# Kernel optimization log

Measured on AMD Instinct MI355X. Metric: run time of the kernel, lower is better.

Reference implementation:

```python
import jax, jax.numpy as jnp
import numpy as np
import math

NUM_EMBED = 1024
EMBED_DIM = 256
COMMITMENT_COST = 0.25


def setup_inputs() -> dict:
    key = jax.random.key(0)
    k1, k2 = jax.random.split(key)
    inputs = jax.random.normal(k1, (16, EMBED_DIM, 4096), dtype=jnp.float32)
    embed = jax.random.normal(k2, (NUM_EMBED, EMBED_DIM), dtype=jnp.float32)
    return {"inputs": inputs, "embed": embed}


def reference(inputs, embed):
    sg = jax.lax.stop_gradient
    num_embed = embed.shape[0]
    # channels-first (B, D, T) -> (B, T, D)
    x = jnp.swapaxes(inputs, 1, -1)
    B, T, D = x.shape
    flat = x.reshape(-1, D)  # (N, D)
    # pairwise squared distances to the codebook: (N, K)
    d2 = (jnp.sum(flat * flat, axis=1, keepdims=True)
          + jnp.sum(embed * embed, axis=1)
          - 2.0 * flat @ embed.T)
    q_idx = jnp.argmin(d2, axis=1)  # (N,) int
    # one-hot @ embed is just a gather of the nearest codewords
    z_q = embed[q_idx].reshape(x.shape)  # (B, T, D)
    vq_loss = jnp.mean((z_q - sg(x)) ** 2)
    commitment_loss = jnp.mean((sg(z_q) - x) ** 2)
    loss = vq_loss + COMMITMENT_COST * commitment_loss
    # straight-through estimator
    z_q_st = x + sg(z_q - x)
    # codebook usage stats: probs = mean of the one-hot rows
    n = flat.shape[0]
    probs = jnp.zeros((num_embed,), dtype=flat.dtype).at[q_idx].add(1.0) / n
    perplexity = jnp.exp(-jnp.sum(probs * jnp.log(probs + 1e-10)))
    num_spatial_positions = n / B  # == T
    kldiv_r = (math.log(num_embed) * num_spatial_positions
               * jnp.ones((B, 1), dtype=x.dtype))
    z_q_out = jnp.swapaxes(z_q_st, 1, -1)  # back to (B, D, T)
    return z_q_out, loss, kldiv_r, perplexity
```

## Files before the change

kernel.cpp:

```cpp
#include <hip/hip_runtime.h>
#include <math.h>

#define T_DIM 4096
#define D_DIM 256
#define K_NUM 1024
#define B_NUM 16
#define N_TOT (B_NUM * T_DIM)
#define EPS_FLAG 0.03f

typedef short short8 __attribute__((ext_vector_type(8)));
typedef float f32x4 __attribute__((ext_vector_type(4)));

#define WS_FLAGCNT 0
#define WS_LOSS 4
#define WS_HIST 64
#define WS_E2 4352
#define WS_QIDX 8704
#define WS_FLAGLIST 270848
#define WS_ESWZ 540672

__device__ inline unsigned short bf16r(float v) {
    unsigned u = __float_as_uint(v);
    unsigned r = u + 0x7FFFu + ((u >> 16) & 1u);
    return (unsigned short)(r >> 16);
}

__device__ inline void gl_lds16(const void* g, void* l) {
    __builtin_amdgcn_global_load_lds(
        (const __attribute__((address_space(1))) unsigned int*)g,
        (__attribute__((address_space(3))) unsigned int*)l, 16, 0, 0);
}

__global__ __launch_bounds__(256) void e2_kernel(const float* __restrict__ embed,
                                                 float* __restrict__ e2) {
    const int wave = threadIdx.x >> 6;
    const int lane = threadIdx.x & 63;
    const int k = blockIdx.x * 4 + wave;
    const float4* row = (const float4*)(embed + (size_t)k * D_DIM);
    float4 v = row[lane];
    float s = v.x * v.x + v.y * v.y + v.z * v.z + v.w * v.w;
    #pragma unroll
    for (int off = 32; off; off >>= 1) s += __shfl_down(s, off);
    if (lane == 0) e2[k] = s;
}

__global__ __launch_bounds__(256) void prep_eswz_kernel(const float* __restrict__ embed,
                                                        unsigned char* __restrict__ eswz) {
    const int tau = blockIdx.x * 256 + threadIdx.x;
    const int g = tau >> 9;
    const int k = (tau >> 6) & 7;
    const int l = tau & 63;
    const int col = g * 16 + (l & 15);
    const int d0 = k * 32 + ((l >> 4) << 3);
    const float* src = embed + (size_t)col * D_DIM + d0;
    short8 hi, lo;
    #pragma unroll
    for (int j = 0; j < 8; ++j) {
        float v = src[j];
        unsigned short hs = bf16r(v);
        float hif = __uint_as_float((unsigned)hs << 16);
        unsigned short ls = bf16r(v - hif);
        hi[j] = (short)hs; lo[j] = (short)ls;
    }
    *(short8*)(eswz + (size_t)g * 16384 + k * 1024 + l * 16) = hi;
    *(short8*)(eswz + (size_t)g * 16384 + 8192 + k * 1024 + l * 16) = lo;
}

__global__ __launch_bounds__(256, 2) void argmin_mfma_kernel(
    const float* __restrict__ x, const unsigned char* __restrict__ eswz,
    const float* __restrict__ e2, int* __restrict__ qidx,
    int* __restrict__ flagcnt, int* __restrict__ flaglist)
{
    __shared__ __align__(16) unsigned char bbuf[2][32768];
    __shared__ float e2s[K_NUM];

    const int tid = threadIdx.x;
    const int w = tid >> 6;
    const int l = tid & 63;
    const int rb = blockIdx.x * 128;
    const int b = rb >> 12;
    const float* xb = x + (size_t)b * (D_DIM * T_DIM);

    {
        const unsigned char* src = eswz + (size_t)tid * 16;
        #pragma unroll
        for (int r = 0; r < 8; ++r) gl_lds16(src + r * 4096, &bbuf[0][tid * 16 + r * 4096]);
    }
    for (int i = tid; i < K_NUM; i += 256) e2s[i] = e2[i];

    short8 Ah[2][8], Al[2][8];
    #pragma unroll
    for (int f = 0; f < 2; ++f) {
        const int row = rb + w * 32 + f * 16 + (l & 15);
        const int t = row & (T_DIM - 1);
        const float* xp = xb + t;
        #pragma unroll
        for (int k = 0; k < 8; ++k) {
            const int d0 = k * 32 + ((l >> 4) << 3);
            short8 hi, lo;
            #pragma unroll
            for (int j = 0; j < 8; ++j) {
                float v = xp[(size_t)(d0 + j) * T_DIM];
                unsigned short hs = bf16r(v);
                float hif = __uint_as_float((unsigned)hs << 16);
                unsigned short ls = bf16r(v - hif);
                hi[j] = (short)hs; lo[j] = (short)ls;
            }
            Ah[f][k] = hi; Al[f][k] = lo;
        }
    }
    __syncthreads();

    float bestv[8], secv[8];
    int   besti[8];
    #pragma unroll
    for (int s = 0; s < 8; ++s) { bestv[s] = 3.4e38f; secv[s] = 3.4e38f; besti[s] = 0x7FFFFFFF; }

    for (int g = 0; g < 32; ++g) {
        if (g + 1 < 32) {
            const unsigned char* src = eswz + (size_t)(g + 1) * 32768 + (size_t)tid * 16;
            unsigned char* dst = &bbuf[(g + 1) & 1][tid * 16];
            #pragma unroll
            for (int r = 0; r < 8; ++r) gl_lds16(src + r * 4096, dst + r * 4096);
        }
        const unsigned char* bb = bbuf[g & 1];

        f32x4 a00 = {0.f,0.f,0.f,0.f}, a01 = {0.f,0.f,0.f,0.f};
        f32x4 a10 = {0.f,0.f,0.f,0.f}, a11 = {0.f,0.f,0.f,0.f};
        #pragma unroll
        for (int k = 0; k < 8; ++k) {
            short8 bh0 = *(const short8*)(bb + k * 1024 + l * 16);
            short8 bl0 = *(const short8*)(bb + 8192 + k * 1024 + l * 16);
            short8 bh1 = *(const short8*)(bb + 16384 + k * 1024 + l * 16);
            short8 bl1 = *(const short8*)(bb + 16384 + 8192 + k * 1024 + l * 16);
            a00 = __builtin_amdgcn_mfma_f32_16x16x32_bf16(Ah[0][k], bh0, a00, 0, 0, 0);
            a10 = __builtin_amdgcn_mfma_f32_16x16x32_bf16(Ah[1][k], bh0, a10, 0, 0, 0);
            a01 = __builtin_amdgcn_mfma_f32_16x16x32_bf16(Ah[0][k], bh1, a01, 0, 0, 0);
            a11 = __builtin_amdgcn_mfma_f32_16x16x32_bf16(Ah[1][k], bh1, a11, 0, 0, 0);
            a00 = __builtin_amdgcn_mfma_f32_16x16x32_bf16(Al[0][k], bh0, a00, 0, 0, 0);
            a10 = __builtin_amdgcn_mfma_f32_16x16x32_bf16(Al[1][k], bh0, a10, 0, 0, 0);
            a01 = __builtin_amdgcn_mfma_f32_16x16x32_bf16(Al[0][k], bh1, a01, 0, 0, 0);
            a11 = __builtin_amdgcn_mfma_f32_16x16x32_bf16(Al[1][k], bh1, a11, 0, 0, 0);
            a00 = __builtin_amdgcn_mfma_f32_16x16x32_bf16(Ah[0][k], bl0, a00, 0, 0, 0);
            a10 = __builtin_amdgcn_mfma_f32_16x16x32_bf16(Ah[1][k], bl0, a10, 0, 0, 0);
            a01 = __builtin_amdgcn_mfma_f32_16x16x32_bf16(Ah[0][k], bl1, a01, 0, 0, 0);
            a11 = __builtin_amdgcn_mfma_f32_16x16x32_bf16(Ah[1][k], bl1, a11, 0, 0, 0);
        }

        const int col0 = g * 32 + (l & 15);
        const float e2a = e2s[col0];
        const float e2b = e2s[col0 + 16];
        #pragma unroll
        for (int f = 0; f < 2; ++f) {
            const f32x4 accA = f ? a10 : a00;
            const f32x4 accB = f ? a11 : a01;
            #pragma unroll
            for (int r = 0; r < 4; ++r) {
                const int s = f * 4 + r;
                float sA = fmaf(-2.f, accA[r], e2a);
                float sB = fmaf(-2.f, accB[r], e2b);
                bool swp = sB < sA;
                float lo = swp ? sB : sA;
                float hi = swp ? sA : sB;
                int   li = swp ? col0 + 16 : col0;
                bool upd = lo < bestv[s];
                float mx = upd ? bestv[s] : lo;
                bestv[s] = upd ? lo : bestv[s];
                besti[s] = upd ? li : besti[s];
                secv[s] = fminf(secv[s], fminf(mx, hi));
            }
        }
        __syncthreads();
    }

    #pragma unroll
    for (int slot = 0; slot < 8; ++slot) {
        float bv = bestv[slot], sv = secv[slot];
        int bi = besti[slot];
        #pragma unroll
        for (int d = 1; d < 16; d <<= 1) {
            float ob = __shfl_xor(bv, d);
            int   oi = __shfl_xor(bi, d);
            float os = __shfl_xor(sv, d);
            bool take = (ob < bv) || (ob == bv && oi < bi);
            float loser = take ? bv : ob;
            bv = take ? ob : bv;
            bi = take ? oi : bi;
            sv = fminf(fminf(sv, os), loser);
        }
        if ((l & 15) == 0) {
            const int row = rb + w * 32 + (slot >> 2) * 16 + (l >> 4) * 4 + (slot & 3);
            qidx[row] = bi;
            if (sv - bv < EPS_FLAG) {
                int p = atomicAdd(flagcnt, 1);
                flaglist[p] = row;
            }
        }
    }
}

__global__ __launch_bounds__(256) void cleanup_kernel(
    const float* __restrict__ x, const float* __restrict__ embed,
    const float* __restrict__ e2, const int* __restrict__ flagcnt,
    const int* __restrict__ flaglist, int* __restrict__ qidx)
{
    __shared__ float xr[256];
    __shared__ float rv[256];
    __shared__ int   rix[256];
    const int tid = threadIdx.x;
    int cnt = flagcnt[0];
    if (cnt > N_TOT) cnt = N_TOT;
    for (int it = blockIdx.x; it < cnt; it += gridDim.x) {
        const int row = flaglist[it];
        const int b = row >> 12, t = row & (T_DIM - 1);
        __syncthreads();
        xr[tid] = x[(size_t)b * (D_DIM * T_DIM) + (size_t)tid * T_DIM + t];
        __syncthreads();
        float best = 3.4e38f; int bi = 0x7FFFFFFF;
        for (int q = 0; q < 4; ++q) {
            const int c = q * 256 + tid;
            const float4* ep = (const float4*)(embed + (size_t)c * D_DIM);
            float acc = 0.f;
            #pragma unroll 8
            for (int dd = 0; dd < 64; ++dd) {
                float4 ev = ep[dd];
                acc = fmaf(ev.x, xr[dd * 4 + 0], acc);
                acc = fmaf(ev.y, xr[dd * 4 + 1], acc);
                acc = fmaf(ev.z, xr[dd * 4 + 2], acc);
                acc = fmaf(ev.w, xr[dd * 4 + 3], acc);
            }
            const float s = e2[c] - 2.f * acc;
            if (s < best || (s == best && c < bi)) { best = s; bi = c; }
        }
        rv[tid] = best; rix[tid] = bi;
        __syncthreads();
        for (int off = 128; off; off >>= 1) {
            if (tid < off) {
                float ov = rv[tid + off]; int oi = rix[tid + off];
                if (ov < rv[tid] || (ov == rv[tid] && oi < rix[tid])) { rv[tid] = ov; rix[tid] = oi; }
            }
            __syncthreads();
        }
        if (tid == 0) qidx[row] = rix[0];
    }
}

__global__ __launch_bounds__(256) void gather_kernel(
    const float* __restrict__ x, const float* __restrict__ embed,
    const int* __restrict__ qidx, float* __restrict__ out,
    float* __restrict__ loss_sum, int* __restrict__ hist)
{
    const int tid = threadIdx.x;
    const int n = blockIdx.x * 256 + tid;
    const int b = n >> 12, t = n & (T_DIM - 1);
    const int d0 = blockIdx.y * 64;
    const int idx = qidx[n];
    if (blockIdx.y == 0) atomicAdd(&hist[idx], 1);

    const float4* ep = (const float4*)(embed + (size_t)idx * D_DIM + d0);
    const float* xp = x + (size_t)b * (D_DIM * T_DIM) + (size_t)d0 * T_DIM + t;
    float*       op = out + (size_t)b * (D_DIM * T_DIM) + (size_t)d0 * T_DIM + t;

    float local = 0.f;
    #pragma unroll 4
    for (int i = 0; i < 16; ++i) {
        const float4 ev = ep[i];
        const size_t dd = (size_t)i * 4;
        float xv0 = xp[(dd + 0) * T_DIM];
        float xv1 = xp[(dd + 1) * T_DIM];
        float xv2 = xp[(dd + 2) * T_DIM];
        float xv3 = xp[(dd + 3) * T_DIM];
        op[(dd + 0) * T_DIM] = ev.x;
        op[(dd + 1) * T_DIM] = ev.y;
        op[(dd + 2) * T_DIM] = ev.z;
        op[(dd + 3) * T_DIM] = ev.w;
        float f0 = ev.x - xv0, f1 = ev.y - xv1, f2 = ev.z - xv2, f3 = ev.w - xv3;
        local = fmaf(f0, f0, local);
        local = fmaf(f1, f1, local);
        local = fmaf(f2, f2, local);
        local = fmaf(f3, f3, local);
    }
    #pragma unroll
    for (int off = 32; off; off >>= 1) local += __shfl_down(local, off);
    __shared__ float ls[4];
    if ((tid & 63) == 0) ls[tid >> 6] = local;
    __syncthreads();
    if (tid == 0) atomicAdd(loss_sum, ls[0] + ls[1] + ls[2] + ls[3]);
}

__global__ __launch_bounds__(256) void finalize_kernel(
    const int* __restrict__ hist, const float* __restrict__ loss_sum,
    float* __restrict__ out)
{
    const int tid = threadIdx.x;
    float acc = 0.f;
    #pragma unroll
    for (int i = tid; i < K_NUM; i += 256) {
        const float p = (float)hist[i] * (1.f / (float)N_TOT);
        acc += p * logf(p + 1e-10f);
    }
    #pragma unroll
    for (int off = 32; off; off >>= 1) acc += __shfl_down(acc, off);
    __shared__ float ls[4];
    if ((tid & 63) == 0) ls[tid >> 6] = acc;
    __syncthreads();
    if (tid == 0) {
        const float H = -(ls[0] + ls[1] + ls[2] + ls[3]);
        const size_t base = (size_t)N_TOT * D_DIM;
        out[base] = 1.25f * loss_sum[0] * (1.f / 16777216.f);
        const float kld = (float)(6.931471805599453 * 4096.0);
        #pragma unroll
        for (int i = 0; i < 16; ++i) out[base + 1 + i] = kld;
        out[base + 17] = expf(H);
    }
}

extern "C" void kernel_launch(void* const* d_in, const int* in_sizes, int n_in,
                              void* d_out, int out_size, void* d_ws, size_t ws_size,
                              hipStream_t stream)
{
    const float* x     = (const float*)d_in[0];
    const float* embed = (const float*)d_in[1];
    float* out = (float*)d_out;

    char* ws = (char*)d_ws;
    int*   flagcnt  = (int*)(ws + WS_FLAGCNT);
    float* loss_sum = (float*)(ws + WS_LOSS);
    int*   hist     = (int*)(ws + WS_HIST);
    float* e2       = (float*)(ws + WS_E2);
    int*   qidx     = (int*)(ws + WS_QIDX);
    int*   flaglist = (int*)(ws + WS_FLAGLIST);
    unsigned char* eswz = (unsigned char*)(ws + WS_ESWZ);

    hipMemsetAsync(ws, 0, 4160, stream);

    e2_kernel<<<K_NUM / 4, 256, 0, stream>>>(embed, e2);
    prep_eswz_kernel<<<128, 256, 0, stream>>>(embed, eswz);
    argmin_mfma_kernel<<<N_TOT / 128, 256, 0, stream>>>(x, eswz, e2, qidx, flagcnt, flaglist);
    cleanup_kernel<<<256, 256, 0, stream>>>(x, embed, e2, flagcnt, flaglist, qidx);
    gather_kernel<<<dim3(N_TOT / 256, 4), 256, 0, stream>>>(x, embed, qidx, out, loss_sum, hist);
    finalize_kernel<<<1, 256, 0, stream>>>(hist, loss_sum, out);
}
```

Baseline: 297.6 us.

## Split codebook across blocks, drop x low-part MFMAs, batch exact cleanup rows

The argmin kernel now covers half the codebook per block via a second grid dimension. It keeps only the bf16 high part of x, so each k-step issues 4 MFMAs instead of 12, and LDS per block is halved to allow 4 blocks per CU. A new merge kernel combines the two partial best/second-best results and flags near-ties, and the flag margin is widened to cover the larger error from dropping x's low part. The cleanup kernel now rescores 16 flagged rows per block with wave-shuffle reductions, which amortises the embedding reads but risks a much longer flag list to process exactly.

```diff
diff --git a/kernel.cpp b/kernel.cpp
--- a/kernel.cpp
+++ b/kernel.cpp
@@ -6,7 +6,7 @@
 #define K_NUM 1024
 #define B_NUM 16
 #define N_TOT (B_NUM * T_DIM)
-#define EPS_FLAG 0.03f
+#define EPS_FLAG 0.4f
 
 typedef short short8 __attribute__((ext_vector_type(8)));
 typedef float f32x4 __attribute__((ext_vector_type(4)));
@@ -17,7 +17,10 @@
 #define WS_E2 4352
 #define WS_QIDX 8704
 #define WS_FLAGLIST 270848
-#define WS_ESWZ 540672
+#define WS_PBV 532992
+#define WS_PSV 1057280
+#define WS_PBI 1581568
+#define WS_ESWZ 2105856
 
 __device__ inline unsigned short bf16r(float v) {
     unsigned u = __float_as_uint(v);
@@ -66,29 +69,31 @@
     *(short8*)(eswz + (size_t)g * 16384 + 8192 + k * 1024 + l * 16) = lo;
 }
 
-__global__ __launch_bounds__(256, 2) void argmin_mfma_kernel(
+__global__ __launch_bounds__(256, 4) void argmin_mfma_kernel(
     const float* __restrict__ x, const unsigned char* __restrict__ eswz,
-    const float* __restrict__ e2, int* __restrict__ qidx,
-    int* __restrict__ flagcnt, int* __restrict__ flaglist)
-{
-    __shared__ __align__(16) unsigned char bbuf[2][32768];
+    const float* __restrict__ e2, float* __restrict__ pbv,
+    float* __restrict__ psv, int* __restrict__ pbi)
+{
+    __shared__ __align__(16) unsigned char bbuf[2][16384];
     __shared__ float e2s[K_NUM];
 
     const int tid = threadIdx.x;
     const int w = tid >> 6;
     const int l = tid & 63;
     const int rb = blockIdx.x * 128;
+    const int h = blockIdx.y;
     const int b = rb >> 12;
     const float* xb = x + (size_t)b * (D_DIM * T_DIM);
+    const unsigned char* ebase = eswz + (size_t)h * 32 * 16384;
 
     {
-        const unsigned char* src = eswz + (size_t)tid * 16;
-        #pragma unroll
-        for (int r = 0; r < 8; ++r) gl_lds16(src + r * 4096, &bbuf[0][tid * 16 + r * 4096]);
+        const unsigned char* src = ebase + (size_t)tid * 16;
+        #pragma unroll
+        for (int r = 0; r < 4; ++r) gl_lds16(src + r * 4096, &bbuf[0][tid * 16 + r * 4096]);
     }
     for (int i = tid; i < K_NUM; i += 256) e2s[i] = e2[i];
 
-    short8 Ah[2][8], Al[2][8];
+    short8 Ah[2][8];
     #pragma unroll
     for (int f = 0; f < 2; ++f) {
         const int row = rb + w * 32 + f * 16 + (l & 15);
@@ -97,16 +102,10 @@
         #pragma unroll
         for (int k = 0; k < 8; ++k) {
             const int d0 = k * 32 + ((l >> 4) << 3);
-            short8 hi, lo;
-            #pragma unroll
-            for (int j = 0; j < 8; ++j) {
-                float v = xp[(size_t)(d0 + j) * T_DIM];
-                unsigned short hs = bf16r(v);
-                float hif = __uint_as_float((unsigned)hs << 16);
-                unsigned short ls = bf16r(v - hif);
-                hi[j] = (short)hs; lo[j] = (short)ls;
-            }
-            Ah[f][k] = hi; Al[f][k] = lo;
+            short8 hi;
+            #pragma unroll
+            for (int j = 0; j < 8; ++j) hi[j] = (short)bf16r(xp[(size_t)(d0 + j) * T_DIM]);
+            Ah[f][k] = hi;
         }
     }
     __syncthreads();
@@ -118,57 +117,38 @@
 
     for (int g = 0; g < 32; ++g) {
         if (g + 1 < 32) {
-            const unsigned char* src = eswz + (size_t)(g + 1) * 32768 + (size_t)tid * 16;
+            const unsigned char* src = ebase + (size_t)(g + 1) * 16384 + (size_t)tid * 16;
             unsigned char* dst = &bbuf[(g + 1) & 1][tid * 16];
             #pragma unroll
-            for (int r = 0; r < 8; ++r) gl_lds16(src + r * 4096, dst + r * 4096);
+            for (int r = 0; r < 4; ++r) gl_lds16(src + r * 4096, dst + r * 4096);
         }
         const unsigned char* bb = bbuf[g & 1];
 
-        f32x4 a00 = {0.f,0.f,0.f,0.f}, a01 = {0.f,0.f,0.f,0.f};
-        f32x4 a10 = {0.f,0.f,0.f,0.f}, a11 = {0.f,0.f,0.f,0.f};
+        f32x4 a0 = {0.f,0.f,0.f,0.f}, a1 = {0.f,0.f,0.f,0.f};
         #pragma unroll
         for (int k = 0; k < 8; ++k) {
-            short8 bh0 = *(const short8*)(bb + k * 1024 + l * 16);
-            short8 bl0 = *(const short8*)(bb + 8192 + k * 1024 + l * 16);
-            short8 bh1 = *(const short8*)(bb + 16384 + k * 1024 + l * 16);
-            short8 bl1 = *(const short8*)(bb + 16384 + 8192 + k * 1024 + l * 16);
-            a00 = __builtin_amdgcn_mfma_f32_16x16x32_bf16(Ah[0][k], bh0, a00, 0, 0, 0);
-            a10 = __builtin_amdgcn_mfma_f32_16x16x32_bf16(Ah[1][k], bh0, a10, 0, 0, 0);
-            a01 = __builtin_amdgcn_mfma_f32_16x16x32_bf16(Ah[0][k], bh1, a01, 0, 0, 0);
-            a11 = __builtin_amdgcn_mfma_f32_16x16x32_bf16(Ah[1][k], bh1, a11, 0, 0, 0);
-            a00 = __builtin_amdgcn_mfma_f32_16x16x32_bf16(Al[0][k], bh0, a00, 0, 0, 0);
-            a10 = __builtin_amdgcn_mfma_f32_16x16x32_bf16(Al[1][k], bh0, a10, 0, 0, 0);
-            a01 = __builtin_amdgcn_mfma_f32_16x16x32_bf16(Al[0][k], bh1, a01, 0, 0, 0);
-            a11 = __builtin_amdgcn_mfma_f32_16x16x32_bf16(Al[1][k], bh1, a11, 0, 0, 0);
-            a00 = __builtin_amdgcn_mfma_f32_16x16x32_bf16(Ah[0][k], bl0, a00, 0, 0, 0);
-            a10 = __builtin_amdgcn_mfma_f32_16x16x32_bf16(Ah[1][k], bl0, a10, 0, 0, 0);
-            a01 = __builtin_amdgcn_mfma_f32_16x16x32_bf16(Ah[0][k], bl1, a01, 0, 0, 0);
-            a11 = __builtin_amdgcn_mfma_f32_16x16x32_bf16(Ah[1][k], bl1, a11, 0, 0, 0);
-        }
-
-        const int col0 = g * 32 + (l & 15);
-        const float e2a = e2s[col0];
-        const float e2b = e2s[col0 + 16];
-        #pragma unroll
-        for (int f = 0; f < 2; ++f) {
-            const f32x4 accA = f ? a10 : a00;
-            const f32x4 accB = f ? a11 : a01;
-            #pragma unroll
-            for (int r = 0; r < 4; ++r) {
-                const int s = f * 4 + r;
-                float sA = fmaf(-2.f, accA[r], e2a);
-                float sB = fmaf(-2.f, accB[r], e2b);
-                bool swp = sB < sA;
-                float lo = swp ? sB : sA;
-                float hi = swp ? sA : sB;
-                int   li = swp ? col0 + 16 : col0;
-                bool upd = lo < bestv[s];
-                float mx = upd ? bestv[s] : lo;
-                bestv[s] = upd ? lo : bestv[s];
-                besti[s] = upd ? li : besti[s];
-                secv[s] = fminf(secv[s], fminf(mx, hi));
-            }
+            short8 bh = *(const short8*)(bb + k * 1024 + l * 16);
+            short8 bl = *(const short8*)(bb + 8192 + k * 1024 + l * 16);
+            a0 = __builtin_amdgcn_mfma_f32_16x16x32_bf16(Ah[0][k], bh, a0, 0, 0, 0);
+            a1 = __builtin_amdgcn_mfma_f32_16x16x32_bf16(Ah[1][k], bh, a1, 0, 0, 0);
+            a0 = __builtin_amdgcn_mfma_f32_16x16x32_bf16(Ah[0][k], bl, a0, 0, 0, 0);
+            a1 = __builtin_amdgcn_mfma_f32_16x16x32_bf16(Ah[1][k], bl, a1, 0, 0, 0);
+        }
+
+        const int col = h * 512 + g * 16 + (l & 15);
+        const float e2c = e2s[col];
+        #pragma unroll
+        for (int r = 0; r < 4; ++r) {
+            float s0 = fmaf(-2.f, a0[r], e2c);
+            bool u0 = s0 < bestv[r];
+            secv[r] = fminf(secv[r], u0 ? bestv[r] : s0);
+            bestv[r] = u0 ? s0 : bestv[r];
+            besti[r] = u0 ? col : besti[r];
+            float s1 = fmaf(-2.f, a1[r], e2c);
+            bool u1 = s1 < bestv[4 + r];
+            secv[4 + r] = fminf(secv[4 + r], u1 ? bestv[4 + r] : s1);
+            bestv[4 + r] = u1 ? s1 : bestv[4 + r];
+            besti[4 + r] = u1 ? col : besti[4 + r];
         }
         __syncthreads();
     }
@@ -190,12 +170,30 @@
         }
         if ((l & 15) == 0) {
             const int row = rb + w * 32 + (slot >> 2) * 16 + (l >> 4) * 4 + (slot & 3);
-            qidx[row] = bi;
-            if (sv - bv < EPS_FLAG) {
-                int p = atomicAdd(flagcnt, 1);
-                flaglist[p] = row;
-            }
-        }
+            const int p = h * N_TOT + row;
+            pbv[p] = bv; psv[p] = sv; pbi[p] = bi;
+        }
+    }
+}
+
+__global__ __launch_bounds__(256) void merge_kernel(
+    const float* __restrict__ pbv, const float* __restrict__ psv,
+    const int* __restrict__ pbi, int* __restrict__ qidx,
+    int* __restrict__ flagcnt, int* __restrict__ flaglist)
+{
+    const int n = blockIdx.x * 256 + threadIdx.x;
+    float b0 = pbv[n], b1 = pbv[N_TOT + n];
+    float s0 = psv[n], s1 = psv[N_TOT + n];
+    int   i0 = pbi[n], i1 = pbi[N_TOT + n];
+    bool take1 = b1 < b0;
+    float bb = take1 ? b1 : b0;
+    int   bi = take1 ? i1 : i0;
+    float loser = take1 ? b0 : b1;
+    float ss = fminf(fminf(s0, s1), loser);
+    qidx[n] = bi;
+    if (ss - bb < EPS_FLAG) {
+        int p = atomicAdd(flagcnt, 1);
+        flaglist[p] = n;
     }
 }
 
@@ -204,44 +202,77 @@
     const float* __restrict__ e2, const int* __restrict__ flagcnt,
     const int* __restrict__ flaglist, int* __restrict__ qidx)
 {
-    __shared__ float xr[256];
-    __shared__ float rv[256];
-    __shared__ int   rix[256];
+    __shared__ float xs[16][256];
+    __shared__ int rows_s[16];
+    __shared__ float rv[16][4];
+    __shared__ int   rix[16][4];
     const int tid = threadIdx.x;
     int cnt = flagcnt[0];
     if (cnt > N_TOT) cnt = N_TOT;
-    for (int it = blockIdx.x; it < cnt; it += gridDim.x) {
-        const int row = flaglist[it];
-        const int b = row >> 12, t = row & (T_DIM - 1);
-        __syncthreads();
-        xr[tid] = x[(size_t)b * (D_DIM * T_DIM) + (size_t)tid * T_DIM + t];
-        __syncthreads();
-        float best = 3.4e38f; int bi = 0x7FFFFFFF;
+    const int ngrp = (cnt + 15) >> 4;
+    for (int grp = blockIdx.x; grp < ngrp; grp += gridDim.x) {
+        __syncthreads();
+        if (tid < 16) rows_s[tid] = (grp * 16 + tid < cnt) ? flaglist[grp * 16 + tid] : -1;
+        __syncthreads();
+        {
+            const int j = tid & 15, ch = tid >> 4;
+            const int row = rows_s[j];
+            if (row >= 0) {
+                const int bb = row >> 12, t = row & (T_DIM - 1);
+                const float* xp = x + (size_t)bb * (D_DIM * T_DIM) + t;
+                #pragma unroll
+                for (int i = 0; i < 16; ++i) {
+                    const int d = ch * 16 + i;
+                    xs[j][d] = xp[(size_t)d * T_DIM];
+                }
+            }
+        }
+        __syncthreads();
+        float bv[16]; int bix[16];
+        #pragma unroll
+        for (int j = 0; j < 16; ++j) { bv[j] = 3.4e38f; bix[j] = 0x7FFFFFFF; }
         for (int q = 0; q < 4; ++q) {
             const int c = q * 256 + tid;
             const float4* ep = (const float4*)(embed + (size_t)c * D_DIM);
-            float acc = 0.f;
-            #pragma unroll 8
-            for (int dd = 0; dd < 64; ++dd) {
-                float4 ev = ep[dd];
-                acc = fmaf(ev.x, xr[dd * 4 + 0], acc);
-                acc = fmaf(ev.y, xr[dd * 4 + 1], acc);
-                acc = fmaf(ev.z, xr[dd * 4 + 2], acc);
-                acc = fmaf(ev.w, xr[dd * 4 + 3], acc);
-            }
-            const float s = e2[c] - 2.f * acc;
-            if (s < best || (s == best && c < bi)) { best = s; bi = c; }
-        }
-        rv[tid] = best; rix[tid] = bi;
-        __syncthreads();
-        for (int off = 128; off; off >>= 1) {
-            if (tid < off) {
-                float ov = rv[tid + off]; int oi = rix[tid + off];
-                if (ov < rv[tid] || (ov == rv[tid] && oi < rix[tid])) { rv[tid] = ov; rix[tid] = oi; }
-            }
-            __syncthreads();
-        }
-        if (tid == 0) qidx[row] = rix[0];
+            float acc[16];
+            #pragma unroll
+            for (int j = 0; j < 16; ++j) acc[j] = 0.f;
+            for (int d4 = 0; d4 < 64; ++d4) {
+                const float4 ev = ep[d4];
+                #pragma unroll
+                for (int j = 0; j < 16; ++j) {
+                    const float4 xv = *(const float4*)&xs[j][d4 * 4];
+                    acc[j] += ev.x * xv.x + ev.y * xv.y + ev.z * xv.z + ev.w * xv.w;
+                }
+            }
+            const float e2c = e2[c];
+            #pragma unroll
+            for (int j = 0; j < 16; ++j) {
+                float s = e2c - 2.f * acc[j];
+                if (s < bv[j] || (s == bv[j] && c < bix[j])) { bv[j] = s; bix[j] = c; }
+            }
+        }
+        const int w = tid >> 6, l = tid & 63;
+        #pragma unroll
+        for (int j = 0; j < 16; ++j) {
+            float v = bv[j]; int i = bix[j];
+            #pragma unroll
+            for (int d = 32; d; d >>= 1) {
+                float ov = __shfl_down(v, d); int oi = __shfl_down(i, d);
+                if (ov < v || (ov == v && oi < i)) { v = ov; i = oi; }
+            }
+            if (l == 0) { rv[j][w] = v; rix[j][w] = i; }
+        }
+        __syncthreads();
+        if (tid < 16 && rows_s[tid] >= 0) {
+            float v = rv[tid][0]; int i = rix[tid][0];
+            #pragma unroll
+            for (int w2 = 1; w2 < 4; ++w2) {
+                float ov = rv[tid][w2]; int oi = rix[tid][w2];
+                if (ov < v || (ov == v && oi < i)) { v = ov; i = oi; }
+            }
+            qidx[rows_s[tid]] = i;
+        }
     }
 }
 
@@ -330,13 +361,17 @@
     float* e2       = (float*)(ws + WS_E2);
     int*   qidx     = (int*)(ws + WS_QIDX);
     int*   flaglist = (int*)(ws + WS_FLAGLIST);
+    float* pbv      = (float*)(ws + WS_PBV);
+    float* psv      = (float*)(ws + WS_PSV);
+    int*   pbi      = (int*)(ws + WS_PBI);
     unsigned char* eswz = (unsigned char*)(ws + WS_ESWZ);
 
     hipMemsetAsync(ws, 0, 4160, stream);
 
     e2_kernel<<<K_NUM / 4, 256, 0, stream>>>(embed, e2);
     prep_eswz_kernel<<<128, 256, 0, stream>>>(embed, eswz);
-    argmin_mfma_kernel<<<N_TOT / 128, 256, 0, stream>>>(x, eswz, e2, qidx, flagcnt, flaglist);
+    argmin_mfma_kernel<<<dim3(N_TOT / 128, 2), 256, 0, stream>>>(x, eswz, e2, pbv, psv, pbi);
+    merge_kernel<<<N_TOT / 256, 256, 0, stream>>>(pbv, psv, pbi, qidx, flagcnt, flaglist);
     cleanup_kernel<<<256, 256, 0, stream>>>(x, embed, e2, flagcnt, flaglist, qidx);
     gather_kernel<<<dim3(N_TOT / 256, 4), 256, 0, stream>>>(x, embed, qidx, out, loss_sum, hist);
     finalize_kernel<<<1, 256, 0, stream>>>(hist, loss_sum, out);
```

Result: slower. 405.1 us (+36.1%).
